# Performance work log

Measured on AMD Instinct MI355X. Metric: run time of the kernel, lower is better.

The kernel has to match this reference:

```python
import jax, jax.numpy as jnp
import numpy as np

EPS = 1e-05


def setup_inputs() -> dict:
    key = jax.random.key(0)
    ks = jax.random.split(key, 7)
    T, d = 8192, 512
    h = jax.random.normal(ks[0], (T, d), dtype=jnp.float32)
    ln_w = jax.random.normal(ks[1], (d,), dtype=jnp.float32) * 0.1
    ln_b = jax.random.normal(ks[2], (d,), dtype=jnp.float32) * 0.1
    w_q = jax.random.normal(ks[3], (d, d), dtype=jnp.float32) * 0.1
    w_k = jax.random.normal(ks[4], (d, d), dtype=jnp.float32) * 0.1
    w_v = jax.random.normal(ks[5], (d, d), dtype=jnp.float32) * 0.1
    w_o = jax.random.normal(ks[6], (d, d), dtype=jnp.float32) * 0.1
    return {"h": h, "ln_w": ln_w, "ln_b": ln_b,
            "w_q": w_q, "w_k": w_k, "w_v": w_v, "w_o": w_o}


def reference(h, ln_w, ln_b, w_q, w_k, w_v, w_o):
    T, d = h.shape
    # LayerNorm (biased variance, matching torch)
    mu = jnp.mean(h, axis=-1, keepdims=True)
    var = jnp.mean(jnp.square(h - mu), axis=-1, keepdims=True)
    h_norm = (h - mu) * jax.lax.rsqrt(var + EPS) * ln_w + ln_b
    # nn.Linear applies x @ W.T
    q = h_norm @ w_q.T  # [T, d]
    k = h_norm @ w_k.T
    v = h_norm @ w_v.T
    scores = (q @ k.T) * (1.0 / jnp.sqrt(jnp.float32(d)))  # [T, T]
    causal = jnp.tril(jnp.ones((T, T), dtype=bool))
    scores = jnp.where(causal, scores, -jnp.inf)
    attn = jax.nn.softmax(scores, axis=-1)
    out = (attn @ v) @ w_o.T
    return h + out
```

## Files before the change

kernel.cpp:

```cpp
#include <hip/hip_runtime.h>
#include <stdint.h>

#define T_SEQ 8192
#define DMODEL 512
#define QKV_LD 1536

typedef __attribute__((ext_vector_type(8))) short bfx8;
typedef __attribute__((ext_vector_type(4))) short bfx4;
typedef __attribute__((ext_vector_type(4))) float fx4;
typedef __attribute__((ext_vector_type(16))) float f32x16;

__device__ __forceinline__ unsigned short f2bf(float f) {
    uint32_t u = __float_as_uint(f);
    u += 0x7fffu + ((u >> 16) & 1u);
    return (unsigned short)(u >> 16);
}
__device__ __forceinline__ float bf2f(unsigned short s) {
    return __uint_as_float(((uint32_t)s) << 16);
}

__device__ __forceinline__ void gload16(const void* g, void* l) {
    __builtin_amdgcn_global_load_lds(
        (const __attribute__((address_space(1))) unsigned int*)g,
        (__attribute__((address_space(3))) unsigned int*)l,
        16, 0, 0);
}

__device__ __forceinline__ void fence_barrier() {
    asm volatile("" ::: "memory");
    __builtin_amdgcn_s_barrier();
    asm volatile("" ::: "memory");
}

__global__ __launch_bounds__(256) void cvt4_bf16_kernel(const float* __restrict__ w0,
                                                        const float* __restrict__ w1,
                                                        const float* __restrict__ w2,
                                                        const float* __restrict__ w3,
                                                        unsigned short* __restrict__ dst) {
    int i = (blockIdx.x * 256 + threadIdx.x) * 8;
    int sel = i >> 18;
    int off = i & 0x3FFFF;
    const float* src = (sel == 0) ? w0 : (sel == 1) ? w1 : (sel == 2) ? w2 : w3;
    fx4 a = *(const fx4*)(src + off);
    fx4 b = *(const fx4*)(src + off + 4);
    bfx8 o;
    o[0] = f2bf(a[0]); o[1] = f2bf(a[1]); o[2] = f2bf(a[2]); o[3] = f2bf(a[3]);
    o[4] = f2bf(b[0]); o[5] = f2bf(b[1]); o[6] = f2bf(b[2]); o[7] = f2bf(b[3]);
    *(bfx8*)(dst + i) = o;
}

__global__ __launch_bounds__(256) void layernorm_kernel(const float* __restrict__ h,
                                                        const float* __restrict__ w,
                                                        const float* __restrict__ b,
                                                        unsigned short* __restrict__ out) {
    int wv = threadIdx.x >> 6, lane = threadIdx.x & 63;
    int row = blockIdx.x * 4 + wv;
    const float* hr = h + (size_t)row * DMODEL + lane * 8;
    fx4 x0 = *(const fx4*)hr;
    fx4 x1 = *(const fx4*)(hr + 4);
    float s  = x0[0]+x0[1]+x0[2]+x0[3]+x1[0]+x1[1]+x1[2]+x1[3];
    float ss = x0[0]*x0[0]+x0[1]*x0[1]+x0[2]*x0[2]+x0[3]*x0[3]
             + x1[0]*x1[0]+x1[1]*x1[1]+x1[2]*x1[2]+x1[3]*x1[3];
    #pragma unroll
    for (int m = 1; m < 64; m <<= 1) { s += __shfl_xor(s, m); ss += __shfl_xor(ss, m); }
    float mu  = s * (1.0f / DMODEL);
    float var = ss * (1.0f / DMODEL) - mu * mu;
    float r = rsqrtf(var + 1e-5f);
    const float* wp = w + lane * 8; const float* bp = b + lane * 8;
    fx4 w0 = *(const fx4*)wp, w1 = *(const fx4*)(wp + 4);
    fx4 b0 = *(const fx4*)bp, b1 = *(const fx4*)(bp + 4);
    bfx8 o;
    o[0] = f2bf((x0[0]-mu)*r*w0[0] + b0[0]);
    o[1] = f2bf((x0[1]-mu)*r*w0[1] + b0[1]);
    o[2] = f2bf((x0[2]-mu)*r*w0[2] + b0[2]);
    o[3] = f2bf((x0[3]-mu)*r*w0[3] + b0[3]);
    o[4] = f2bf((x1[0]-mu)*r*w1[0] + b1[0]);
    o[5] = f2bf((x1[1]-mu)*r*w1[1] + b1[1]);
    o[6] = f2bf((x1[2]-mu)*r*w1[2] + b1[2]);
    o[7] = f2bf((x1[3]-mu)*r*w1[3] + b1[3]);
    *(bfx8*)(out + (size_t)row * DMODEL + lane * 8) = o;
}

template<int RESID>
__global__ __launch_bounds__(256, 2) void gemm_bt_kernel(
    const unsigned short* __restrict__ A,
    const unsigned short* __restrict__ B,
    unsigned short* __restrict__ Cb,
    float* __restrict__ Cf,
    const float* __restrict__ resid,
    int M, int N, int K)
{
    __shared__ unsigned short At[128 * 64];
    __shared__ unsigned short Bt[128 * 64];
    int tid = threadIdx.x;
    int wv = tid >> 6, lane = tid & 63, l15 = lane & 15, l4 = lane >> 4;
    int wr = wv >> 1, wc = wv & 1;
    int row0 = blockIdx.y * 128;
    int col0 = blockIdx.x * 128;
    fx4 acc[4][4] = {};
    const char* Abase = (const char*)(A + (size_t)row0 * K);
    const char* Bbase = (const char*)(B + (size_t)col0 * K);
    for (int kt = 0; kt < K; kt += 64) {
        #pragma unroll
        for (int ch = 0; ch < 4; ch++) {
            int bix = (ch * 256 + tid) * 16;
            int r = bix >> 7;
            int sb = (bix & 127) ^ ((r & 7) << 4);
            bfx8 va = *(const bfx8*)(Abase + (size_t)r * (K * 2) + kt * 2 + sb);
            bfx8 vb = *(const bfx8*)(Bbase + (size_t)r * (K * 2) + kt * 2 + sb);
            *(bfx8*)((char*)At + bix) = va;
            *(bfx8*)((char*)Bt + bix) = vb;
        }
        __syncthreads();
        #pragma unroll
        for (int ks = 0; ks < 2; ks++) {
            bfx8 af[4], bf[4];
            #pragma unroll
            for (int m = 0; m < 4; m++) {
                int ra = wr * 64 + m * 16 + l15;
                int ka = (ks * 64 + l4 * 16) ^ ((ra & 7) << 4);
                af[m] = *(const bfx8*)((const char*)At + ra * 128 + ka);
                int rb = wc * 64 + m * 16 + l15;
                int kb = (ks * 64 + l4 * 16) ^ ((rb & 7) << 4);
                bf[m] = *(const bfx8*)((const char*)Bt + rb * 128 + kb);
            }
            #pragma unroll
            for (int m = 0; m < 4; m++)
                #pragma unroll
                for (int n = 0; n < 4; n++)
                    acc[m][n] = __builtin_amdgcn_mfma_f32_16x16x32_bf16(af[m], bf[n], acc[m][n], 0, 0, 0);
        }
        __syncthreads();
    }
    #pragma unroll
    for (int m = 0; m < 4; m++)
        #pragma unroll
        for (int n = 0; n < 4; n++)
            #pragma unroll
            for (int r = 0; r < 4; r++) {
                int row = row0 + wr * 64 + m * 16 + l4 * 4 + r;
                int col = col0 + wc * 64 + n * 16 + l15;
                float v = acc[m][n][r];
                size_t o = (size_t)row * N + col;
                if (RESID) Cf[o] = v + resid[o];
                else       Cb[o] = f2bf(v);
            }
}

__global__ __launch_bounds__(256) void transpose_kernel(const unsigned short* __restrict__ v,
                                                        unsigned short* __restrict__ vt, int ld) {
    __shared__ unsigned short tile[64][80];
    int t = threadIdx.x;
    int r0 = blockIdx.x * 64;
    int c0 = blockIdx.y * 64;
    int r = t >> 2, cw = (t & 3) * 16;
    const unsigned short* src = v + (size_t)(r0 + r) * ld + c0 + cw;
    bfx8 a = *(const bfx8*)src;
    bfx8 b = *(const bfx8*)(src + 8);
    #pragma unroll
    for (int j = 0; j < 8; j++) { tile[r][cw + j] = a[j]; tile[r][cw + 8 + j] = b[j]; }
    __syncthreads();
    int dc = t >> 2, rb = (t & 3) * 16;
    bfx8 o0, o1;
    #pragma unroll
    for (int j = 0; j < 8; j++) { o0[j] = tile[rb + j][dc]; o1[j] = tile[rb + 8 + j][dc]; }
    unsigned short* dst = vt + (size_t)(c0 + dc) * T_SEQ + r0 + rb;
    *(bfx8*)dst = o0;
    *(bfx8*)(dst + 8) = o1;
}

__global__ __launch_bounds__(768)
void flash15_kernel(
    const unsigned short* __restrict__ q,
    const unsigned short* __restrict__ k,
    const unsigned short* __restrict__ vt,
    unsigned short* __restrict__ opart,
    float* __restrict__ mbuf, float* __restrict__ lbuf,
    int CH, int NBLK)
{
    __shared__ unsigned short Q_lds[64 * 512];
    __shared__ unsigned short K_lds[32 * 512];
    __shared__ unsigned short V_lds[512 * 32];
    __shared__ unsigned short Sp_lds[2 * 64 * 32];
    __shared__ unsigned short p_lds[64 * 32];
    __shared__ float alpha_lds[64];

    int tid = threadIdx.x;
    int wv = tid >> 6, lane = tid & 63, l15 = lane & 15, l4 = lane >> 4;
    int l31 = lane & 31, hi = lane >> 5;
    bool isS = wv < 4;

    int L = blockIdx.x;
    int bid = (L & 7) * (NBLK >> 3) + (L >> 3);

    int c = 0;
    while (bid >= 128 * (c + 1) - CH * (c + 1) * c / 2) c++;
    int qi = CH * c + (bid - (128 * c - CH * c * (c - 1) / 2));
    int R0 = qi * 64;
    int kv_begin = c * CH * 64;
    int kv_end = min(kv_begin + CH * 64, R0 + 64);
    int ntile = (kv_end - kv_begin) >> 5;

    int qg = wv >> 1, kb = wv & 1;
    int ro = (wv - 4) >> 2, co = (wv - 4) & 3;

    const float rscale = 0.044194173824159216f;

    float m_run = -INFINITY, l_run = 0.f;
    int srow = wv * 16 + (lane >> 2);
    fx4 acc[2][8] = {};

    uint32_t koff[4], voff[4];
    {
        #pragma unroll
        for (int j = 0; j < 4; j++) {
            int krow = wv * 4 + j;
            koff[j] = (uint32_t)krow * (QKV_LD * 2) + ((lane * 16) ^ ((krow & 15) << 4));
            int seg = (wv - 4) * 4 + j;
            int r = seg * 8 + (lane >> 3);
            int pg = lane & 7;
            int lg = pg ^ (r & 7);
            int d = 2 * r + ((lg >> 2) & 1);
            int ch = lg & 3;
            voff[j] = (uint32_t)d * (T_SEQ * 2) + ch * 16;
        }
    }
    const char* kbase = (const char*)k + (size_t)kv_begin * (QKV_LD * 2);
    const char* vbase = (const char*)vt + (size_t)kv_begin * 2;

    auto stageQ = [&]() {
        if (wv >= 8) return;
        const char* qb = (const char*)q + (size_t)R0 * (QKV_LD * 2);
        #pragma unroll
        for (int j = 0; j < 8; j++) {
            int row = wv * 8 + j;
            const char* gp = qb + (size_t)row * (QKV_LD * 2)
                           + ((lane * 16) ^ ((row & 15) << 4));
            gload16(gp, (char*)Q_lds + row * 1024);
        }
    };
    auto stageK2 = [&](const char* kb2) {
        if (wv >= 8) return;
        #pragma unroll
        for (int j = 0; j < 4; j++)
            gload16(kb2 + koff[j], (char*)K_lds + (wv * 4 + j) * 1024);
    };
    auto stageV2 = [&](const char* vb2) {
        if (wv < 4) return;
        #pragma unroll
        for (int j = 0; j < 4; j++)
            gload16(vb2 + voff[j], (char*)V_lds + ((wv - 4) * 4 + j) * 1024);
    };

    stageQ();
    stageK2(kbase);

    for (int t = 0; t <= ntile; t++) {
        int kv0 = kv_begin + t * 32;

        asm volatile("s_waitcnt vmcnt(0)" ::: "memory");
        fence_barrier();
        __builtin_amdgcn_sched_barrier(0);

        if (isS) {
            if (t < ntile) {
                f32x16 sacc = {};
                int ksw = (l31 & 15) << 4;
                int qrow = qg * 32 + l31;
                int qsw = (qrow & 15) << 4;
                const char* kbase2 = (const char*)K_lds + l31 * 1024;
                const char* qbase2 = (const char*)Q_lds + qrow * 1024;
                #pragma unroll
                for (int ks = 0; ks < 16; ks++) {
                    int off = kb * 512 + ks * 32 + hi * 16;
                    bfx8 kfr = *(const bfx8*)(kbase2 + (off ^ ksw));
                    bfx8 qfr = *(const bfx8*)(qbase2 + (off ^ qsw));
                    sacc = __builtin_amdgcn_mfma_f32_32x32x16_bf16(kfr, qfr, sacc, 0, 0, 0);
                }
                char* spb = (char*)Sp_lds + kb * 4096 + qrow * 64;
                int spsw = (qrow & 3) << 4;
                #pragma unroll
                for (int a = 0; a < 4; a++) {
                    bfx4 ch;
                    #pragma unroll
                    for (int b = 0; b < 4; b++) {
                        int r = a * 4 + b;
                        int kvloc = b + 8 * a + 4 * hi;
                        float x = sacc[r] * rscale;
                        if (kv0 + kvloc > R0 + qrow) x = -INFINITY;
                        ch[b] = (short)f2bf(x);
                    }
                    *(bfx4*)(spb + ((a * 16 + hi * 8) ^ spsw)) = ch;
                }
            }
        } else {
            if (t > 0) {
                fx4 apv[2];
                apv[0] = *(const fx4*)&alpha_lds[ro * 32 + l4 * 4];
                apv[1] = *(const fx4*)&alpha_lds[ro * 32 + 16 + l4 * 4];
                bool need = !(apv[0][0] == 1.f && apv[0][1] == 1.f && apv[0][2] == 1.f && apv[0][3] == 1.f
                           && apv[1][0] == 1.f && apv[1][1] == 1.f && apv[1][2] == 1.f && apv[1][3] == 1.f);
                if (__any(need)) {
                    #pragma unroll
                    for (int m = 0; m < 2; m++)
                        #pragma unroll
                        for (int n = 0; n < 8; n++)
                            #pragma unroll
                            for (int r = 0; r < 4; r++)
                                acc[m][n][r] *= apv[m][r];
                }
                bfx8 pa[2];
                #pragma unroll
                for (int m = 0; m < 2; m++) {
                    int prow = ro * 32 + m * 16 + l15;
                    int pr = prow >> 1;
                    int ppg = (((prow & 1) << 2) | l4) ^ (pr & 7);
                    pa[m] = *(const bfx8*)((const char*)p_lds + pr * 128 + ppg * 16);
                }
                #pragma unroll
                for (int n = 0; n < 8; n++) {
                    int d = co * 128 + n * 16 + l15;
                    int vr = d >> 1;
                    int vpg = (((d & 1) << 2) | l4) ^ (vr & 7);
                    bfx8 vfr = *(const bfx8*)((const char*)V_lds + vr * 128 + vpg * 16);
                    acc[0][n] = __builtin_amdgcn_mfma_f32_16x16x32_bf16(pa[0], vfr, acc[0][n], 0, 0, 0);
                    acc[1][n] = __builtin_amdgcn_mfma_f32_16x16x32_bf16(pa[1], vfr, acc[1][n], 0, 0, 0);
                }
            }
        }
        if (t == ntile) break;

        asm volatile("s_waitcnt lgkmcnt(0)" ::: "memory");
        fence_barrier();
        __builtin_amdgcn_sched_barrier(0);

        if (t + 1 < ntile) stageK2(kbase + (size_t)(t + 1) * 32 * (QKV_LD * 2));
        stageV2(vbase + (size_t)t * 64);

        if (isS) {
            int soff = srow * 64 + (((lane & 3) * 16) ^ ((srow & 3) << 4));
            bfx8 s0 = *(const bfx8*)((const char*)Sp_lds + soff);
            bfx8 s1 = *(const bfx8*)((const char*)Sp_lds + 4096 + soff);
            float xv[8];
            float mx = -INFINITY;
            #pragma unroll
            for (int j = 0; j < 8; j++) {
                xv[j] = bf2f((unsigned short)s0[j]) + bf2f((unsigned short)s1[j]);
                mx = fmaxf(mx, xv[j]);
            }
            mx = fmaxf(mx, __shfl_xor(mx, 1));
            mx = fmaxf(mx, __shfl_xor(mx, 2));
            float al;
            if (__all(mx <= m_run)) {
                al = 1.f;
            } else {
                float mn = fmaxf(m_run, mx);
                float msafe = (mn == -INFINITY) ? 0.f : mn;
                al = __expf(m_run - msafe);
                m_run = mn;
            }
            float msafe2 = (m_run == -INFINITY) ? 0.f : m_run;
            if ((lane & 3) == 0) alpha_lds[srow] = al;
            float ps = 0.f;
            bfx8 pw;
            #pragma unroll
            for (int j = 0; j < 8; j++) {
                float p = __expf(xv[j] - msafe2);
                pw[j] = (short)f2bf(p);
                ps += p;
            }
            {
                int pr = srow >> 1;
                int ppg = (((srow & 1) << 2) | (lane & 3)) ^ (pr & 7);
                *(bfx8*)((char*)p_lds + pr * 128 + ppg * 16) = pw;
            }
            ps += __shfl_xor(ps, 1);
            ps += __shfl_xor(ps, 2);
            l_run = l_run * al + ps;
        }
    }

    if (!isS) {
        #pragma unroll
        for (int m = 0; m < 2; m++)
            #pragma unroll
            for (int n = 0; n < 8; n++)
                #pragma unroll
                for (int r = 0; r < 4; r++) {
                    int rowl = ro * 32 + m * 16 + l4 * 4 + r;
                    int col = co * 128 + n * 16 + l15;
                    opart[((size_t)bid * 64 + rowl) * DMODEL + col] = f2bf(acc[m][n][r]);
                }
    } else if ((lane & 3) == 0) {
        mbuf[(size_t)bid * 64 + srow] = m_run;
        lbuf[(size_t)bid * 64 + srow] = l_run;
    }
}

__global__ __launch_bounds__(256) void combine2_kernel(
    const unsigned short* __restrict__ opart,
    const float* __restrict__ mbuf, const float* __restrict__ lbuf,
    unsigned short* __restrict__ attn, int CH)
{
    int tid = threadIdx.x;
    int row = blockIdx.x * 4 + (tid >> 6);
    int col = (tid & 63) * 8;
    int qi = row >> 6, rowl = row & 63;
    int nch = qi / CH + 1;
    float M = -INFINITY;
    for (int c = 0; c < nch; c++) {
        int pidx = 128 * c - CH * c * (c - 1) / 2 + (qi - CH * c);
        M = fmaxf(M, mbuf[(size_t)pidx * 64 + rowl]);
    }
    float L = 0.f;
    float accv[8] = {0.f,0.f,0.f,0.f,0.f,0.f,0.f,0.f};
    for (int c = 0; c < nch; c++) {
        int pidx = 128 * c - CH * c * (c - 1) / 2 + (qi - CH * c);
        float e = __expf(mbuf[(size_t)pidx * 64 + rowl] - M);
        L += lbuf[(size_t)pidx * 64 + rowl] * e;
        bfx8 v = *(const bfx8*)(opart + ((size_t)pidx * 64 + rowl) * DMODEL + col);
        #pragma unroll
        for (int j = 0; j < 8; j++) accv[j] += e * bf2f((unsigned short)v[j]);
    }
    float invL = 1.0f / L;
    bfx8 o;
    #pragma unroll
    for (int j = 0; j < 8; j++) o[j] = f2bf(accv[j] * invL);
    *(bfx8*)(attn + (size_t)row * DMODEL + col) = o;
}

extern "C" void kernel_launch(void* const* d_in, const int* in_sizes, int n_in,
                              void* d_out, int out_size, void* d_ws, size_t ws_size,
                              hipStream_t stream) {
    const float* h   = (const float*)d_in[0];
    const float* lnw = (const float*)d_in[1];
    const float* lnb = (const float*)d_in[2];
    const float* wq  = (const float*)d_in[3];
    const float* wk  = (const float*)d_in[4];
    const float* wv  = (const float*)d_in[5];
    const float* wo  = (const float*)d_in[6];
    float* out = (float*)d_out;

    char* ws = (char*)d_ws;
    size_t off = 0;
    auto alloc = [&](size_t bytes) {
        char* p = ws + off;
        off += (bytes + 255) & ~(size_t)255;
        return p;
    };
    const size_t TD2 = (size_t)T_SEQ * DMODEL * 2;
    const size_t W2  = (size_t)DMODEL * DMODEL * 2;
    unsigned short* hn   = (unsigned short*)alloc(TD2);
    unsigned short* wall = (unsigned short*)alloc(4 * W2);
    unsigned short* wqkv = wall;
    unsigned short* wob  = wall + 3 * DMODEL * DMODEL;
    unsigned short* qkvb = (unsigned short*)alloc((size_t)T_SEQ * QKV_LD * 2);
    unsigned short* vtb  = (unsigned short*)alloc(TD2);
    unsigned short* attnb= (unsigned short*)alloc(TD2);

    int CH = 8, NBLK = 1088;
    {
        size_t need = off + 2 * ((1088u * 64 * 4 + 255) & ~(size_t)255)
                    + (((size_t)1088 * 64 * 512 * 2 + 255) & ~(size_t)255);
        if (need > ws_size) { CH = 16; NBLK = 576; }
    }
    float* mbuf = (float*)alloc((size_t)NBLK * 64 * 4);
    float* lbuf = (float*)alloc((size_t)NBLK * 64 * 4);
    unsigned short* opart = (unsigned short*)alloc((size_t)NBLK * 64 * 512 * 2);

    cvt4_bf16_kernel<<<dim3(512), dim3(256), 0, stream>>>(wq, wk, wv, wo, wall);

    layernorm_kernel<<<dim3(T_SEQ / 4), dim3(256), 0, stream>>>(h, lnw, lnb, hn);

    gemm_bt_kernel<0><<<dim3(QKV_LD / 128, T_SEQ / 128), dim3(256), 0, stream>>>(
        hn, wqkv, qkvb, nullptr, nullptr, T_SEQ, QKV_LD, DMODEL);

    transpose_kernel<<<dim3(T_SEQ / 64, DMODEL / 64), dim3(256), 0, stream>>>(
        qkvb + 2 * DMODEL, vtb, QKV_LD);

    flash15_kernel<<<dim3(NBLK), dim3(768), 0, stream>>>(
        qkvb, qkvb + DMODEL, vtb, opart, mbuf, lbuf, CH, NBLK);

    combine2_kernel<<<dim3(T_SEQ / 4), dim3(256), 0, stream>>>(opart, mbuf, lbuf, attnb, CH);

    gemm_bt_kernel<1><<<dim3(DMODEL / 128, T_SEQ / 128), dim3(256), 0, stream>>>(
        attnb, wob, nullptr, out, h, T_SEQ, DMODEL, DMODEL);
}
```

Measured before the change: 250.4 us.

## Keep Q fragments in registers and double-buffer K/V tiles in LDS

The flash attention kernel drops the Q tile from LDS. Each score wave loads its Q fragments once into registers (16 bfx8). The freed LDS holds double-buffered K and V tiles, and K is prefetched two tiles ahead. The single full vmcnt(0) wait becomes partial waits, so global loads overlap with compute, and all K/V loading moves to the four PV waves. The cost is higher VGPR pressure in the score waves and a heavier load burden on the PV waves.

```diff
diff --git a/kernel.cpp b/kernel.cpp
--- a/kernel.cpp
+++ b/kernel.cpp
@@ -170,7 +170,7 @@
 }
 
 __global__ __launch_bounds__(768)
-void flash15_kernel(
+void flash16_kernel(
     const unsigned short* __restrict__ q,
     const unsigned short* __restrict__ k,
     const unsigned short* __restrict__ vt,
@@ -178,9 +178,8 @@
     float* __restrict__ mbuf, float* __restrict__ lbuf,
     int CH, int NBLK)
 {
-    __shared__ unsigned short Q_lds[64 * 512];
-    __shared__ unsigned short K_lds[32 * 512];
-    __shared__ unsigned short V_lds[512 * 32];
+    __shared__ unsigned short K_lds[2][32 * 512];
+    __shared__ unsigned short V_lds[2][512 * 32];
     __shared__ unsigned short Sp_lds[2 * 64 * 32];
     __shared__ unsigned short p_lds[64 * 32];
     __shared__ float alpha_lds[64];
@@ -210,55 +209,49 @@
     int srow = wv * 16 + (lane >> 2);
     fx4 acc[2][8] = {};
 
-    uint32_t koff[4], voff[4];
-    {
+    bfx8 qf[16];
+    if (isS) {
+        const unsigned short* qp = q + (size_t)(R0 + qg * 32 + l31) * QKV_LD + kb * 256 + hi * 8;
+        #pragma unroll
+        for (int ks = 0; ks < 16; ks++) qf[ks] = *(const bfx8*)(qp + ks * 16);
+    }
+
+    auto stageK = [&](int t2) {
+        if (wv < 4) return;
+        const char* kbp = (const char*)k + ((size_t)kv_begin + (size_t)t2 * 32) * (QKV_LD * 2);
         #pragma unroll
         for (int j = 0; j < 4; j++) {
-            int krow = wv * 4 + j;
-            koff[j] = (uint32_t)krow * (QKV_LD * 2) + ((lane * 16) ^ ((krow & 15) << 4));
+            int krow = (wv - 4) * 4 + j;
+            const char* gp = kbp + (size_t)krow * (QKV_LD * 2) + ((lane * 16) ^ ((krow & 15) << 4));
+            gload16(gp, (char*)K_lds[t2 & 1] + krow * 1024);
+        }
+    };
+    auto stageV = [&](int t2) {
+        if (wv < 4) return;
+        const char* vb = (const char*)vt + ((size_t)kv_begin + (size_t)t2 * 32) * 2;
+        #pragma unroll
+        for (int j = 0; j < 4; j++) {
             int seg = (wv - 4) * 4 + j;
             int r = seg * 8 + (lane >> 3);
             int pg = lane & 7;
             int lg = pg ^ (r & 7);
             int d = 2 * r + ((lg >> 2) & 1);
-            int ch = lg & 3;
-            voff[j] = (uint32_t)d * (T_SEQ * 2) + ch * 16;
-        }
-    }
-    const char* kbase = (const char*)k + (size_t)kv_begin * (QKV_LD * 2);
-    const char* vbase = (const char*)vt + (size_t)kv_begin * 2;
-
-    auto stageQ = [&]() {
-        if (wv >= 8) return;
-        const char* qb = (const char*)q + (size_t)R0 * (QKV_LD * 2);
-        #pragma unroll
-        for (int j = 0; j < 8; j++) {
-            int row = wv * 8 + j;
-            const char* gp = qb + (size_t)row * (QKV_LD * 2)
-                           + ((lane * 16) ^ ((row & 15) << 4));
-            gload16(gp, (char*)Q_lds + row * 1024);
+            int ch2 = lg & 3;
+            const char* gp = vb + (size_t)d * (T_SEQ * 2) + ch2 * 16;
+            gload16(gp, (char*)V_lds[t2 & 1] + seg * 1024);
         }
     };
-    auto stageK2 = [&](const char* kb2) {
-        if (wv >= 8) return;
-        #pragma unroll
-        for (int j = 0; j < 4; j++)
-            gload16(kb2 + koff[j], (char*)K_lds + (wv * 4 + j) * 1024);
-    };
-    auto stageV2 = [&](const char* vb2) {
-        if (wv < 4) return;
-        #pragma unroll
-        for (int j = 0; j < 4; j++)
-            gload16(vb2 + voff[j], (char*)V_lds + ((wv - 4) * 4 + j) * 1024);
-    };
-
-    stageQ();
-    stageK2(kbase);
+
+    stageK(0);
+    if (ntile > 1) stageK(1);
+    stageV(0);
 
     for (int t = 0; t <= ntile; t++) {
         int kv0 = kv_begin + t * 32;
 
-        asm volatile("s_waitcnt vmcnt(0)" ::: "memory");
+        if (t == ntile)          asm volatile("s_waitcnt vmcnt(0)" ::: "memory");
+        else if (t + 1 == ntile) asm volatile("s_waitcnt vmcnt(4)" ::: "memory");
+        else                     asm volatile("s_waitcnt vmcnt(8)" ::: "memory");
         fence_barrier();
         __builtin_amdgcn_sched_barrier(0);
 
@@ -266,17 +259,13 @@
             if (t < ntile) {
                 f32x16 sacc = {};
                 int ksw = (l31 & 15) << 4;
+                const char* kbase2 = (const char*)K_lds[t & 1] + l31 * 1024;
+                #pragma unroll
+                for (int ks = 0; ks < 16; ks++) {
+                    bfx8 kfr = *(const bfx8*)(kbase2 + ((kb * 512 + ks * 32 + hi * 16) ^ ksw));
+                    sacc = __builtin_amdgcn_mfma_f32_32x32x16_bf16(kfr, qf[ks], sacc, 0, 0, 0);
+                }
                 int qrow = qg * 32 + l31;
-                int qsw = (qrow & 15) << 4;
-                const char* kbase2 = (const char*)K_lds + l31 * 1024;
-                const char* qbase2 = (const char*)Q_lds + qrow * 1024;
-                #pragma unroll
-                for (int ks = 0; ks < 16; ks++) {
-                    int off = kb * 512 + ks * 32 + hi * 16;
-                    bfx8 kfr = *(const bfx8*)(kbase2 + (off ^ ksw));
-                    bfx8 qfr = *(const bfx8*)(qbase2 + (off ^ qsw));
-                    sacc = __builtin_amdgcn_mfma_f32_32x32x16_bf16(kfr, qfr, sacc, 0, 0, 0);
-                }
                 char* spb = (char*)Sp_lds + kb * 4096 + qrow * 64;
                 int spsw = (qrow & 3) << 4;
                 #pragma unroll
@@ -317,12 +306,13 @@
                     int ppg = (((prow & 1) << 2) | l4) ^ (pr & 7);
                     pa[m] = *(const bfx8*)((const char*)p_lds + pr * 128 + ppg * 16);
                 }
+                const char* vbuf = (const char*)V_lds[(t - 1) & 1];
                 #pragma unroll
                 for (int n = 0; n < 8; n++) {
                     int d = co * 128 + n * 16 + l15;
                     int vr = d >> 1;
                     int vpg = (((d & 1) << 2) | l4) ^ (vr & 7);
-                    bfx8 vfr = *(const bfx8*)((const char*)V_lds + vr * 128 + vpg * 16);
+                    bfx8 vfr = *(const bfx8*)(vbuf + vr * 128 + vpg * 16);
                     acc[0][n] = __builtin_amdgcn_mfma_f32_16x16x32_bf16(pa[0], vfr, acc[0][n], 0, 0, 0);
                     acc[1][n] = __builtin_amdgcn_mfma_f32_16x16x32_bf16(pa[1], vfr, acc[1][n], 0, 0, 0);
                 }
@@ -334,8 +324,8 @@
         fence_barrier();
         __builtin_amdgcn_sched_barrier(0);
 
-        if (t + 1 < ntile) stageK2(kbase + (size_t)(t + 1) * 32 * (QKV_LD * 2));
-        stageV2(vbase + (size_t)t * 64);
+        if (t + 2 < ntile) stageK(t + 2);
+        if (t + 1 < ntile) stageV(t + 1);
 
         if (isS) {
             int soff = srow * 64 + (((lane & 3) * 16) ^ ((srow & 3) << 4));
@@ -478,7 +468,7 @@
     transpose_kernel<<<dim3(T_SEQ / 64, DMODEL / 64), dim3(256), 0, stream>>>(
         qkvb + 2 * DMODEL, vtb, QKV_LD);
 
-    flash15_kernel<<<dim3(NBLK), dim3(768), 0, stream>>>(
+    flash16_kernel<<<dim3(NBLK), dim3(768), 0, stream>>>(
         qkvb, qkvb + DMODEL, vtb, opart, mbuf, lbuf, CH, NBLK);
 
     combine2_kernel<<<dim3(T_SEQ / 4), dim3(256), 0, stream>>>(opart, mbuf, lbuf, attnb, CH);
```

New measurement: 395.6 us. +58.0%, slower.
